# Kernel optimization log

Measured on AMD Instinct MI355X. Metric: run time of the kernel, lower is better.

Reference implementation:

```python
import jax, jax.numpy as jnp
import numpy as np

D_MODEL = 1024
D_STATE = 16
D_CONV = 4
EXPAND = 2
D_INNER = EXPAND * D_MODEL  # 2048
DT_RANK = (D_MODEL + 15) // 16  # 64
BATCH = 2
SEQ = 1024


def setup_inputs() -> dict:
    key = jax.random.key(0)
    ks = jax.random.split(key, 9)
    s = 0.02
    x = jax.random.normal(ks[0], (BATCH, SEQ, D_MODEL), jnp.float32)
    W_in = jax.random.normal(ks[1], (D_MODEL, 2 * D_INNER), jnp.float32) * s
    conv_w = jax.random.normal(ks[2], (D_INNER, D_CONV), jnp.float32) * s
    conv_b = jnp.zeros((D_INNER,), jnp.float32)
    W_x = jax.random.normal(ks[3], (D_INNER, DT_RANK + 2 * D_STATE), jnp.float32) * s
    W_dt = jax.random.normal(ks[4], (DT_RANK, D_INNER), jnp.float32) * (DT_RANK ** -0.5)
    # dt bias init: inverse softplus of dt ~ U(1e-3, 0.1)
    dt0 = jax.random.uniform(ks[5], (D_INNER,), jnp.float32, 1e-3, 0.1)
    b_dt = dt0 + jnp.log(-jnp.expm1(-dt0))
    # S4D-real A init: A[d, n] = -(n+1)
    A_log = jnp.log(jnp.tile(jnp.arange(1, D_STATE + 1, dtype=jnp.float32), (D_INNER, 1)))
    D_skip = jnp.ones((D_INNER,), jnp.float32)
    W_out = jax.random.normal(ks[6], (D_INNER, D_MODEL), jnp.float32) * s
    return {"x": x, "W_in": W_in, "conv_w": conv_w, "conv_b": conv_b,
            "W_x": W_x, "W_dt": W_dt, "b_dt": b_dt, "A_log": A_log,
            "D_skip": D_skip, "W_out": W_out}


def _mamba_forward(x, W_in, conv_w, conv_b, W_x, W_dt, b_dt, A_log, D_skip, W_out):
    Bsz, L, _ = x.shape
    # input projection -> [B, L, 2*d_inner], split into stream and gate
    xz = x @ W_in
    xr, z = jnp.split(xz, 2, axis=-1)
    # depthwise causal conv1d over time
    xt = xr.transpose(0, 2, 1)                       # [B, d_inner, L]
    kern = conv_w[:, None, :]                        # [d_inner, 1, d_conv]
    xc = jax.lax.conv_general_dilated(
        xt, kern, window_strides=(1,), padding=[(D_CONV - 1, 0)],
        feature_group_count=D_INNER, dimension_numbers=("NCH", "OIH", "NCH"))
    xc = jax.nn.silu(xc + conv_b[None, :, None]).transpose(0, 2, 1)  # [B, L, d_inner]
    # data-dependent dt, B, C
    dbl = xc @ W_x                                   # [B, L, dt_rank + 2*d_state]
    dt, Bm, Cm = jnp.split(dbl, [DT_RANK, DT_RANK + D_STATE], axis=-1)
    dt = jax.nn.softplus(dt @ W_dt + b_dt)           # [B, L, d_inner]
    A = -jnp.exp(A_log)                              # [d_inner, d_state]

    def step(h, inp):
        dt_t, B_t, C_t, x_t = inp                    # [B,d_inner],[B,d_state],[B,d_state],[B,d_inner]
        dA = jnp.exp(dt_t[..., None] * A)            # [B, d_inner, d_state]
        h = dA * h + (dt_t * x_t)[..., None] * B_t[:, None, :]
        y = jnp.einsum("bds,bs->bd", h, C_t)
        return h, y

    h0 = jnp.zeros((Bsz, D_INNER, D_STATE), x.dtype)
    xs = (dt.transpose(1, 0, 2), Bm.transpose(1, 0, 2),
          Cm.transpose(1, 0, 2), xc.transpose(1, 0, 2))
    _, ys = jax.lax.scan(step, h0, xs)               # ys: [L, B, d_inner]
    y = ys.transpose(1, 0, 2) + xc * D_skip
    y = y * jax.nn.silu(z)
    return y @ W_out                                 # [B, L, d_model]


def reference(x, W_in, conv_w, conv_b, W_x, W_dt, b_dt, A_log, D_skip, W_out):
    return _mamba_forward(x, W_in, conv_w, conv_b, W_x, W_dt, b_dt, A_log, D_skip, W_out)
```

## Files before the change

kernel.cpp:

```cpp
#include <hip/hip_runtime.h>

#define BATCH 2
#define SEQL 1024
#define DMODEL 1024
#define DINNER 2048
#define DSTATE 16
#define DTRANK 64
#define NCH 64
#define LC 16

typedef short bf16x8 __attribute__((ext_vector_type(8)));
typedef float f32x4 __attribute__((ext_vector_type(4)));
typedef int i32x4 __attribute__((ext_vector_type(4)));

__device__ __forceinline__ unsigned short f2bf(float f) {
  unsigned u = __float_as_uint(f);
  return (unsigned short)((u + 0x7fffu + ((u >> 16) & 1u)) >> 16);
}
__device__ __forceinline__ float bf2f(unsigned short u) {
  return __uint_as_float((unsigned)u << 16);
}
__device__ __forceinline__ float sigmoidf_(float x) { return 1.f / (1.f + __expf(-x)); }

__device__ __forceinline__ void gl_lds16(const unsigned short* g, unsigned short* l) {
  __builtin_amdgcn_global_load_lds(
      (const __attribute__((address_space(1))) unsigned int*)g,
      (__attribute__((address_space(3))) unsigned int*)l, 16, 0, 0);
}

#define BM 128
#define BN 128

__global__ __launch_bounds__(256) void k_gemm_mfma(
    const unsigned short* __restrict__ A,
    const unsigned short* __restrict__ Bt,
    float* __restrict__ C, unsigned short* __restrict__ C2,
    int M, int N, int K, const float* __restrict__ bias, int mode)
{
  __shared__ __attribute__((aligned(16))) unsigned short As[128 * 64];
  __shared__ __attribute__((aligned(16))) unsigned short Bs[128 * 64];
  const int tid = threadIdx.x;
  const int wave = tid >> 6, lane = tid & 63;
  const int m0 = blockIdx.x * BM, n0 = blockIdx.y * BN;
  const int Kc = K / gridDim.z;
  const int k0beg = blockIdx.z * Kc;
  float* Cz = C + (size_t)blockIdx.z * M * N;
  const int wr = (wave >> 1) * 64, wc = (wave & 1) * 64;
  const int fr = lane & 15;
  const int qw = lane >> 4;

  int srow[4], scol[4];
  #pragma unroll
  for (int i = 0; i < 4; ++i) {
    int off = wave * 4096 + i * 1024 + lane * 16;
    int row = off >> 7;
    int c16 = ((off >> 4) & 7) ^ (row & 7);
    srow[i] = row;
    scol[i] = c16 * 8;
  }

  f32x4 acc[4][4] = {};
  for (int k0 = k0beg; k0 < k0beg + Kc; k0 += 64) {
    #pragma unroll
    for (int i = 0; i < 4; ++i)
      gl_lds16(A + (size_t)(m0 + srow[i]) * K + k0 + scol[i],
               &As[(wave * 4096 + i * 1024) >> 1]);
    #pragma unroll
    for (int i = 0; i < 4; ++i)
      gl_lds16(Bt + (size_t)(n0 + srow[i]) * K + k0 + scol[i],
               &Bs[(wave * 4096 + i * 1024) >> 1]);
    __syncthreads();
    #pragma unroll
    for (int t = 0; t < 2; ++t) {
      bf16x8 af[4], bfv[4];
      #pragma unroll
      for (int i = 0; i < 4; ++i) {
        int row = wr + i * 16 + fr;
        int c16 = (t * 4 + qw) ^ (row & 7);
        af[i] = *(const bf16x8*)&As[row * 64 + c16 * 8];
      }
      #pragma unroll
      for (int j = 0; j < 4; ++j) {
        int row = wc + j * 16 + fr;
        int c16 = (t * 4 + qw) ^ (row & 7);
        bfv[j] = *(const bf16x8*)&Bs[row * 64 + c16 * 8];
      }
      #pragma unroll
      for (int i = 0; i < 4; ++i)
        #pragma unroll
        for (int j = 0; j < 4; ++j)
          acc[i][j] = __builtin_amdgcn_mfma_f32_16x16x32_bf16(af[i], bfv[j], acc[i][j], 0, 0, 0);
    }
    __syncthreads();
  }
  const int rr = qw * 4;
  if (mode == 1) {
    #pragma unroll
    for (int j = 0; j < 4; ++j) {
      float bj = bias[n0 + wc + j * 16 + fr];
      #pragma unroll
      for (int i = 0; i < 4; ++i)
        #pragma unroll
        for (int r = 0; r < 4; ++r) {
          float v = acc[i][j][r] + bj;
          C2[(size_t)(m0 + wr + i * 16 + rr + r) * N + (n0 + wc + j * 16 + fr)] =
              f2bf(__logf(1.f + __expf(v)));
        }
    }
  } else if (mode == 2) {
    if (n0 < 2048) {
      #pragma unroll
      for (int i = 0; i < 4; ++i)
        #pragma unroll
        for (int j = 0; j < 4; ++j)
          #pragma unroll
          for (int r = 0; r < 4; ++r)
            C[(size_t)(m0 + wr + i * 16 + rr + r) * 2048 + (n0 + wc + j * 16 + fr)] =
                acc[i][j][r];
    } else {
      #pragma unroll
      for (int i = 0; i < 4; ++i)
        #pragma unroll
        for (int j = 0; j < 4; ++j)
          #pragma unroll
          for (int r = 0; r < 4; ++r)
            C2[(size_t)(m0 + wr + i * 16 + rr + r) * 2048 + (n0 - 2048 + wc + j * 16 + fr)] =
                f2bf(acc[i][j][r]);
    }
  } else {
    #pragma unroll
    for (int i = 0; i < 4; ++i)
      #pragma unroll
      for (int j = 0; j < 4; ++j)
        #pragma unroll
        for (int r = 0; r < 4; ++r)
          Cz[(size_t)(m0 + wr + i * 16 + rr + r) * N + (n0 + wc + j * 16 + fr)] = acc[i][j][r];
  }
}

__device__ __forceinline__ void transpose_tile(
    const float* __restrict__ src, unsigned short* __restrict__ dst,
    int R, int C, int bx, int by, float* t )
{
  int bc = bx * 64, br = by * 64;
  int tr = threadIdx.x >> 2;
  int tc = (threadIdx.x & 3) * 16;
  #pragma unroll
  for (int i = 0; i < 4; ++i) {
    float4 v = *(const float4*)(src + (size_t)(br + tr) * C + bc + tc + i * 4);
    t[tr * 65 + tc + i * 4 + 0] = v.x; t[tr * 65 + tc + i * 4 + 1] = v.y;
    t[tr * 65 + tc + i * 4 + 2] = v.z; t[tr * 65 + tc + i * 4 + 3] = v.w;
  }
  __syncthreads();
  unsigned short tmp[16];
  #pragma unroll
  for (int i = 0; i < 16; ++i) tmp[i] = f2bf(t[(tc + i) * 65 + tr]);
  unsigned short* dp = dst + (size_t)(bc + tr) * R + br + tc;
  *(i32x4*)dp = *(i32x4*)&tmp[0];
  *(i32x4*)(dp + 8) = *(i32x4*)&tmp[8];
}

__global__ __launch_bounds__(256) void k_prep(
    const float* __restrict__ x,   unsigned short* __restrict__ xbf,
    const float* __restrict__ Win, unsigned short* __restrict__ wint,
    const float* __restrict__ Wout,unsigned short* __restrict__ woutt,
    const float* __restrict__ Wdt, unsigned short* __restrict__ wdtt,
    const float* __restrict__ Wx,  unsigned short* __restrict__ wxt)
{
  __shared__ float t[64 * 65];
  int bid = blockIdx.x;
  if (bid < 1024) {
    int i = (bid * 256 + threadIdx.x) * 8;
    float4 a = *(const float4*)(x + i);
    float4 b = *(const float4*)(x + i + 4);
    unsigned short tmp[8] = {f2bf(a.x), f2bf(a.y), f2bf(a.z), f2bf(a.w),
                             f2bf(b.x), f2bf(b.y), f2bf(b.z), f2bf(b.w)};
    *(i32x4*)(xbf + i) = *(i32x4*)tmp;
  } else if (bid < 2048) {
    int tt = bid - 1024;
    transpose_tile(Win, wint, 1024, 4096, tt & 63, tt >> 6, t);
  } else if (bid < 2560) {
    int tt = bid - 2048;
    transpose_tile(Wout, woutt, 2048, 1024, tt & 15, tt >> 4, t);
  } else if (bid < 2592) {
    int tt = bid - 2560;
    transpose_tile(Wdt, wdtt, 64, 2048, tt, 0, t);
  } else {
    int idx = (bid - 2592) * 256 + threadIdx.x;
    int k = idx & (DINNER - 1);
    int n = idx >> 11;
    float v = (n < 96) ? Wx[(size_t)k * 96 + n] : 0.f;
    wxt[idx] = f2bf(v);
  }
}

__global__ __launch_bounds__(256) void k_conv_silu(
    const float* __restrict__ xr, const float* __restrict__ cw,
    const float* __restrict__ cb, unsigned short* __restrict__ xcb)
{
  int idx = blockIdx.x * 256 + threadIdx.x;
  int d = idx & (DINNER - 1);
  int bl = idx >> 11;
  int l = bl & (SEQL - 1);
  float s = cb[d];
  #pragma unroll
  for (int k = 0; k < 4; ++k) {
    int ll = l - 3 + k;
    if (ll >= 0) s += xr[(size_t)(bl - 3 + k) * DINNER + d] * cw[d * 4 + k];
  }
  float r = s * sigmoidf_(s);
  xcb[idx] = f2bf(r);
}

__global__ void k_reduce2(const float* __restrict__ part, float* __restrict__ dbl,
                          unsigned short* __restrict__ dtraw)
{
  int idx = blockIdx.x * 256 + threadIdx.x;
  float s = 0.f;
  #pragma unroll
  for (int z = 0; z < 16; ++z) s += part[(size_t)z * 2048 * 128 + idx];
  dbl[idx] = s;
  int col = idx & 127, rw = idx >> 7;
  if (col < 64) dtraw[rw * 64 + col] = f2bf(s);
}

__global__ void k_reduce5(const float* __restrict__ part, float* __restrict__ out)
{
  int idx = (blockIdx.x * 256 + threadIdx.x) * 4;
  f32x4 s = *(const f32x4*)(part + idx);
  #pragma unroll
  for (int z = 1; z < 4; ++z)
    s += *(const f32x4*)(part + (size_t)z * 2048 * 1024 + idx);
  *(f32x4*)(out + idx) = s;
}

__global__ __launch_bounds__(256) void k_scan_A(
    const unsigned short* __restrict__ dtb, const unsigned short* __restrict__ xcb,
    const float* __restrict__ dbl, const float* __restrict__ Alog,
    float2* __restrict__ hpair)
{
  __shared__ __attribute__((aligned(16))) float bcB[LC][DSTATE];
  int gid = blockIdx.x * 256 + threadIdx.x;
  int d = gid & (DINNER - 1);
  int t = gid >> 11;
  int c = t & (NCH - 1);
  int b = t >> 6;
  const int r0 = b * SEQL + c * LC;
  bcB[threadIdx.x >> 4][threadIdx.x & 15] =
      dbl[(size_t)(r0 + (threadIdx.x >> 4)) * 128 + 64 + (threadIdx.x & 15)];
  float As[DSTATE];
  #pragma unroll
  for (int i = 0; i < 4; ++i) {
    f32x4 a = *(const f32x4*)&Alog[d * DSTATE + i * 4];
    #pragma unroll
    for (int j = 0; j < 4; ++j) As[i * 4 + j] = -__expf(a[j]);
  }
  __syncthreads();
  float h[DSTATE];
  #pragma unroll
  for (int s = 0; s < DSTATE; ++s) h[s] = 0.f;
  float sumdt = 0.f;
  #pragma unroll
  for (int li = 0; li < LC; li += 2) {
    float dt0 = bf2f(dtb[(size_t)(r0 + li) * DINNER + d]);
    float xv0 = bf2f(xcb[(size_t)(r0 + li) * DINNER + d]);
    float dt1 = bf2f(dtb[(size_t)(r0 + li + 1) * DINNER + d]);
    float xv1 = bf2f(xcb[(size_t)(r0 + li + 1) * DINNER + d]);
    f32x4 B0[4], B1[4];
    #pragma unroll
    for (int i = 0; i < 4; ++i) B0[i] = *(const f32x4*)&bcB[li][i * 4];
    #pragma unroll
    for (int i = 0; i < 4; ++i) B1[i] = *(const f32x4*)&bcB[li + 1][i * 4];
    float dtx0 = dt0 * xv0, dtx1 = dt1 * xv1;
    sumdt += dt0 + dt1;
    const float* Bv0 = (const float*)B0;
    const float* Bv1 = (const float*)B1;
    #pragma unroll
    for (int s = 0; s < DSTATE; ++s) {
      float dA0 = __expf(dt0 * As[s]);
      h[s] = dA0 * h[s] + dtx0 * Bv0[s];
      float dA1 = __expf(dt1 * As[s]);
      h[s] = dA1 * h[s] + dtx1 * Bv1[s];
    }
  }
  size_t base = ((size_t)(b * NCH + c) * DSTATE) * DINNER + d;
  #pragma unroll
  for (int s = 0; s < DSTATE; ++s) {
    float2 v; v.x = h[s]; v.y = __expf(sumdt * As[s]);
    hpair[base + (size_t)s * DINNER] = v;
  }
}

__global__ void k_scan_B(const float2* __restrict__ hpair, float* __restrict__ hin)
{
  int gid = blockIdx.x * 256 + threadIdx.x;
  int d = gid & (DINNER - 1);
  int s = (gid >> 11) & (DSTATE - 1);
  int b = gid >> 15;
  float h = 0.f;
  for (int c0 = 0; c0 < NCH; c0 += 8) {
    float2 v[8];
    #pragma unroll
    for (int i = 0; i < 8; ++i)
      v[i] = hpair[((size_t)(b * NCH + c0 + i) * DSTATE + s) * DINNER + d];
    #pragma unroll
    for (int i = 0; i < 8; ++i) {
      hin[((size_t)(b * NCH + c0 + i) * DSTATE + s) * DINNER + d] = h;
      h = v[i].y * h + v[i].x;
    }
  }
}

__global__ __launch_bounds__(256) void k_scan_C(
    const unsigned short* __restrict__ dtb, const unsigned short* __restrict__ xcb,
    const float* __restrict__ dbl, const float* __restrict__ Alog,
    const float* __restrict__ hin, const float* __restrict__ Dskip,
    const unsigned short* __restrict__ zb, unsigned short* __restrict__ yact)
{
  __shared__ __attribute__((aligned(16))) float bc[LC][32];
  int gid = blockIdx.x * 256 + threadIdx.x;
  int d = gid & (DINNER - 1);
  int t = gid >> 11;
  int c = t & (NCH - 1);
  int b = t >> 6;
  const int r0 = b * SEQL + c * LC;
  {
    int step = threadIdx.x >> 4, j = (threadIdx.x & 15) * 2;
    float2 v = *(const float2*)&dbl[(size_t)(r0 + step) * 128 + 64 + j];
    bc[step][j] = v.x; bc[step][j + 1] = v.y;
  }
  float As[DSTATE];
  #pragma unroll
  for (int i = 0; i < 4; ++i) {
    f32x4 a = *(const f32x4*)&Alog[d * DSTATE + i * 4];
    #pragma unroll
    for (int j = 0; j < 4; ++j) As[i * 4 + j] = -__expf(a[j]);
  }
  float h[DSTATE];
  size_t base = ((size_t)(b * NCH + c) * DSTATE) * DINNER + d;
  #pragma unroll
  for (int s = 0; s < DSTATE; ++s) h[s] = hin[base + (size_t)s * DINNER];
  const float dsk = Dskip[d];
  __syncthreads();
  #pragma unroll
  for (int li = 0; li < LC; li += 2) {
    const int r = r0 + li;
    float dt0 = bf2f(dtb[(size_t)r * DINNER + d]);
    float xv0 = bf2f(xcb[(size_t)r * DINNER + d]);
    float zv0 = bf2f(zb [(size_t)r * DINNER + d]);
    float dt1 = bf2f(dtb[(size_t)(r + 1) * DINNER + d]);
    float xv1 = bf2f(xcb[(size_t)(r + 1) * DINNER + d]);
    float zv1 = bf2f(zb [(size_t)(r + 1) * DINNER + d]);
    f32x4 B0[4], C0[4], B1[4], C1[4];
    #pragma unroll
    for (int i = 0; i < 4; ++i) B0[i] = *(const f32x4*)&bc[li][i * 4];
    #pragma unroll
    for (int i = 0; i < 4; ++i) C0[i] = *(const f32x4*)&bc[li][16 + i * 4];
    #pragma unroll
    for (int i = 0; i < 4; ++i) B1[i] = *(const f32x4*)&bc[li + 1][i * 4];
    #pragma unroll
    for (int i = 0; i < 4; ++i) C1[i] = *(const f32x4*)&bc[li + 1][16 + i * 4];
    const float* Bv0 = (const float*)B0; const float* Cv0 = (const float*)C0;
    const float* Bv1 = (const float*)B1; const float* Cv1 = (const float*)C1;
    float dtx0 = dt0 * xv0, dtx1 = dt1 * xv1;
    float y0 = 0.f, y1 = 0.f;
    #pragma unroll
    for (int s = 0; s < DSTATE; ++s) {
      float dA0 = __expf(dt0 * As[s]);
      h[s] = dA0 * h[s] + dtx0 * Bv0[s];
      y0 += h[s] * Cv0[s];
      float dA1 = __expf(dt1 * As[s]);
      h[s] = dA1 * h[s] + dtx1 * Bv1[s];
      y1 += h[s] * Cv1[s];
    }
    y0 += xv0 * dsk;
    y1 += xv1 * dsk;
    float ya0 = y0 * (zv0 * sigmoidf_(zv0));
    float ya1 = y1 * (zv1 * sigmoidf_(zv1));
    yact[(size_t)r * DINNER + d] = f2bf(ya0);
    yact[(size_t)(r + 1) * DINNER + d] = f2bf(ya1);
  }
}

extern "C" void kernel_launch(void* const* d_in, const int* in_sizes, int n_in,
                              void* d_out, int out_size, void* d_ws, size_t ws_size,
                              hipStream_t stream) {
  const float* x     = (const float*)d_in[0];
  const float* Win   = (const float*)d_in[1];
  const float* cw    = (const float*)d_in[2];
  const float* cbias = (const float*)d_in[3];
  const float* Wx    = (const float*)d_in[4];
  const float* Wdt   = (const float*)d_in[5];
  const float* bdt   = (const float*)d_in[6];
  const float* Alog  = (const float*)d_in[7];
  const float* Dsk   = (const float*)d_in[8];
  const float* Wout  = (const float*)d_in[9];
  float* out = (float*)d_out;

  char* ws = (char*)d_ws;
  const size_t MB = 1 << 20;
  float*          xr    = (float*)         (ws);
  unsigned short* xbf   = (unsigned short*)(ws + 16 * MB);
  unsigned short* wint  = (unsigned short*)(ws + 20 * MB);
  unsigned short* xcb   = (unsigned short*)(ws + 28 * MB);
  unsigned short* wxt   = (unsigned short*)(ws + 36 * MB);
  float*          dbl   = (float*)         (ws + 37 * MB);
  unsigned short* dtraw = (unsigned short*)(ws + 38 * MB);
  unsigned short* wdtt  = (unsigned short*)(ws + 39 * MB);
  unsigned short* dtb16 = (unsigned short*)(ws + 40 * MB);
  unsigned short* zb    = (unsigned short*)(ws + 48 * MB);
  float2*         hpair = (float2*)        (ws + 56 * MB);
  float*          hin   = (float*)         (ws + 88 * MB);
  unsigned short* yact  = (unsigned short*)(ws + 104 * MB);
  unsigned short* woutt = (unsigned short*)(ws + 112 * MB);
  float* part2 = (float*)(ws);
  float* part5 = (float*)(ws);
  (void)ws_size; (void)in_sizes; (void)n_in; (void)out_size;

  k_prep<<<3616, 256, 0, stream>>>(x, xbf, Win, wint, Wout, woutt, Wdt, wdtt, Wx, wxt);
  k_gemm_mfma<<<dim3(16, 32, 1), 256, 0, stream>>>(xbf, wint, xr, zb, 2048, 4096, 1024, nullptr, 2);
  k_conv_silu<<<16384, 256, 0, stream>>>(xr, cw, cbias, xcb);
  k_gemm_mfma<<<dim3(16, 1, 16), 256, 0, stream>>>(xcb, wxt, part2, nullptr, 2048, 128, 2048, nullptr, 0);
  k_reduce2<<<1024, 256, 0, stream>>>(part2, dbl, dtraw);
  k_gemm_mfma<<<dim3(16, 16, 1), 256, 0, stream>>>(dtraw, wdtt, nullptr, dtb16, 2048, 2048, 64, bdt, 1);
  k_scan_A<<<1024, 256, 0, stream>>>(dtb16, xcb, dbl, Alog, hpair);
  k_scan_B<<<256, 256, 0, stream>>>(hpair, hin);
  k_scan_C<<<1024, 256, 0, stream>>>(dtb16, xcb, dbl, Alog, hin, Dsk, zb, yact);
  k_gemm_mfma<<<dim3(16, 8, 4), 256, 0, stream>>>(yact, woutt, part5, nullptr, 2048, 1024, 2048, nullptr, 0);
  k_reduce5<<<2048, 256, 0, stream>>>(part5, out);
}
```

Baseline: 151.5 us.

## Store whole in-projection output as bf16 and use longer scan chunks

The in-projection GEMM now writes both the x and z halves as one bf16 [rows, 4096] buffer instead of fp32 x plus bf16 z. The conv and scan_C kernels read from that interleaved buffer. The chunked scan moves from 64 chunks of 16 steps to 32 chunks of 32 steps, which halves the chunk-state traffic and the work in the sequential pass, at the cost of fewer blocks and a partly unrolled inner loop. The workspace layout is reorganized to match. Rounding the conv input to bf16 adds some precision loss.

```diff
diff --git a/kernel.cpp b/kernel.cpp
--- a/kernel.cpp
+++ b/kernel.cpp
@@ -6,8 +6,8 @@
 #define DINNER 2048
 #define DSTATE 16
 #define DTRANK 64
-#define NCH 64
-#define LC 16
+#define NCH 32
+#define LC 32
 
 typedef short bf16x8 __attribute__((ext_vector_type(8)));
 typedef float f32x4 __attribute__((ext_vector_type(4)));
@@ -108,25 +108,14 @@
         }
     }
   } else if (mode == 2) {
-    if (n0 < 2048) {
-      #pragma unroll
-      for (int i = 0; i < 4; ++i)
+    #pragma unroll
+    for (int i = 0; i < 4; ++i)
+      #pragma unroll
+      for (int j = 0; j < 4; ++j)
         #pragma unroll
-        for (int j = 0; j < 4; ++j)
-          #pragma unroll
-          for (int r = 0; r < 4; ++r)
-            C[(size_t)(m0 + wr + i * 16 + rr + r) * 2048 + (n0 + wc + j * 16 + fr)] =
-                acc[i][j][r];
-    } else {
-      #pragma unroll
-      for (int i = 0; i < 4; ++i)
-        #pragma unroll
-        for (int j = 0; j < 4; ++j)
-          #pragma unroll
-          for (int r = 0; r < 4; ++r)
-            C2[(size_t)(m0 + wr + i * 16 + rr + r) * 2048 + (n0 - 2048 + wc + j * 16 + fr)] =
-                f2bf(acc[i][j][r]);
-    }
+        for (int r = 0; r < 4; ++r)
+          C2[(size_t)(m0 + wr + i * 16 + rr + r) * N + (n0 + wc + j * 16 + fr)] =
+              f2bf(acc[i][j][r]);
   } else {
     #pragma unroll
     for (int i = 0; i < 4; ++i)
@@ -195,7 +184,7 @@
 }
 
 __global__ __launch_bounds__(256) void k_conv_silu(
-    const float* __restrict__ xr, const float* __restrict__ cw,
+    const unsigned short* __restrict__ xzb, const float* __restrict__ cw,
     const float* __restrict__ cb, unsigned short* __restrict__ xcb)
 {
   int idx = blockIdx.x * 256 + threadIdx.x;
@@ -206,7 +195,7 @@
   #pragma unroll
   for (int k = 0; k < 4; ++k) {
     int ll = l - 3 + k;
-    if (ll >= 0) s += xr[(size_t)(bl - 3 + k) * DINNER + d] * cw[d * 4 + k];
+    if (ll >= 0) s += bf2f(xzb[(size_t)(bl - 3 + k) * 4096 + d]) * cw[d * 4 + k];
   }
   float r = s * sigmoidf_(s);
   xcb[idx] = f2bf(r);
@@ -244,10 +233,12 @@
   int d = gid & (DINNER - 1);
   int t = gid >> 11;
   int c = t & (NCH - 1);
-  int b = t >> 6;
+  int b = t >> 5;
   const int r0 = b * SEQL + c * LC;
-  bcB[threadIdx.x >> 4][threadIdx.x & 15] =
-      dbl[(size_t)(r0 + (threadIdx.x >> 4)) * 128 + 64 + (threadIdx.x & 15)];
+  for (int i = threadIdx.x; i < LC * DSTATE; i += 256) {
+    int step = i >> 4, col = i & 15;
+    bcB[step][col] = dbl[(size_t)(r0 + step) * 128 + 64 + col];
+  }
   float As[DSTATE];
   #pragma unroll
   for (int i = 0; i < 4; ++i) {
@@ -260,7 +251,7 @@
   #pragma unroll
   for (int s = 0; s < DSTATE; ++s) h[s] = 0.f;
   float sumdt = 0.f;
-  #pragma unroll
+  #pragma unroll 4
   for (int li = 0; li < LC; li += 2) {
     float dt0 = bf2f(dtb[(size_t)(r0 + li) * DINNER + d]);
     float xv0 = bf2f(xcb[(size_t)(r0 + li) * DINNER + d]);
@@ -315,19 +306,18 @@
     const unsigned short* __restrict__ dtb, const unsigned short* __restrict__ xcb,
     const float* __restrict__ dbl, const float* __restrict__ Alog,
     const float* __restrict__ hin, const float* __restrict__ Dskip,
-    const unsigned short* __restrict__ zb, unsigned short* __restrict__ yact)
+    const unsigned short* __restrict__ xzb, unsigned short* __restrict__ yact)
 {
   __shared__ __attribute__((aligned(16))) float bc[LC][32];
   int gid = blockIdx.x * 256 + threadIdx.x;
   int d = gid & (DINNER - 1);
   int t = gid >> 11;
   int c = t & (NCH - 1);
-  int b = t >> 6;
+  int b = t >> 5;
   const int r0 = b * SEQL + c * LC;
-  {
-    int step = threadIdx.x >> 4, j = (threadIdx.x & 15) * 2;
-    float2 v = *(const float2*)&dbl[(size_t)(r0 + step) * 128 + 64 + j];
-    bc[step][j] = v.x; bc[step][j + 1] = v.y;
+  for (int i = threadIdx.x; i < LC * 32; i += 256) {
+    int step = i >> 5, j = i & 31;
+    bc[step][j] = dbl[(size_t)(r0 + step) * 128 + 64 + j];
   }
   float As[DSTATE];
   #pragma unroll
@@ -342,15 +332,15 @@
   for (int s = 0; s < DSTATE; ++s) h[s] = hin[base + (size_t)s * DINNER];
   const float dsk = Dskip[d];
   __syncthreads();
-  #pragma unroll
+  #pragma unroll 4
   for (int li = 0; li < LC; li += 2) {
     const int r = r0 + li;
     float dt0 = bf2f(dtb[(size_t)r * DINNER + d]);
     float xv0 = bf2f(xcb[(size_t)r * DINNER + d]);
-    float zv0 = bf2f(zb [(size_t)r * DINNER + d]);
+    float zv0 = bf2f(xzb[(size_t)r * 4096 + 2048 + d]);
     float dt1 = bf2f(dtb[(size_t)(r + 1) * DINNER + d]);
     float xv1 = bf2f(xcb[(size_t)(r + 1) * DINNER + d]);
-    float zv1 = bf2f(zb [(size_t)(r + 1) * DINNER + d]);
+    float zv1 = bf2f(xzb[(size_t)(r + 1) * 4096 + 2048 + d]);
     f32x4 B0[4], C0[4], B1[4], C1[4];
     #pragma unroll
     for (int i = 0; i < 4; ++i) B0[i] = *(const f32x4*)&bc[li][i * 4];
@@ -399,7 +389,7 @@
 
   char* ws = (char*)d_ws;
   const size_t MB = 1 << 20;
-  float*          xr    = (float*)         (ws);
+  unsigned short* xzb   = (unsigned short*)(ws);
   unsigned short* xbf   = (unsigned short*)(ws + 16 * MB);
   unsigned short* wint  = (unsigned short*)(ws + 20 * MB);
   unsigned short* xcb   = (unsigned short*)(ws + 28 * MB);
@@ -408,24 +398,23 @@
   unsigned short* dtraw = (unsigned short*)(ws + 38 * MB);
   unsigned short* wdtt  = (unsigned short*)(ws + 39 * MB);
   unsigned short* dtb16 = (unsigned short*)(ws + 40 * MB);
-  unsigned short* zb    = (unsigned short*)(ws + 48 * MB);
-  float2*         hpair = (float2*)        (ws + 56 * MB);
-  float*          hin   = (float*)         (ws + 88 * MB);
-  unsigned short* yact  = (unsigned short*)(ws + 104 * MB);
-  unsigned short* woutt = (unsigned short*)(ws + 112 * MB);
-  float* part2 = (float*)(ws);
-  float* part5 = (float*)(ws);
+  float2*         hpair = (float2*)        (ws + 48 * MB);
+  float*          hin   = (float*)         (ws + 64 * MB);
+  unsigned short* yact  = (unsigned short*)(ws + 72 * MB);
+  unsigned short* woutt = (unsigned short*)(ws + 80 * MB);
+  float*          part2 = (float*)         (ws + 84 * MB);
+  float*          part5 = (float*)         (ws + 100 * MB);
   (void)ws_size; (void)in_sizes; (void)n_in; (void)out_size;
 
   k_prep<<<3616, 256, 0, stream>>>(x, xbf, Win, wint, Wout, woutt, Wdt, wdtt, Wx, wxt);
-  k_gemm_mfma<<<dim3(16, 32, 1), 256, 0, stream>>>(xbf, wint, xr, zb, 2048, 4096, 1024, nullptr, 2);
-  k_conv_silu<<<16384, 256, 0, stream>>>(xr, cw, cbias, xcb);
+  k_gemm_mfma<<<dim3(16, 32, 1), 256, 0, stream>>>(xbf, wint, nullptr, xzb, 2048, 4096, 1024, nullptr, 2);
+  k_conv_silu<<<16384, 256, 0, stream>>>(xzb, cw, cbias, xcb);
   k_gemm_mfma<<<dim3(16, 1, 16), 256, 0, stream>>>(xcb, wxt, part2, nullptr, 2048, 128, 2048, nullptr, 0);
   k_reduce2<<<1024, 256, 0, stream>>>(part2, dbl, dtraw);
   k_gemm_mfma<<<dim3(16, 16, 1), 256, 0, stream>>>(dtraw, wdtt, nullptr, dtb16, 2048, 2048, 64, bdt, 1);
-  k_scan_A<<<1024, 256, 0, stream>>>(dtb16, xcb, dbl, Alog, hpair);
+  k_scan_A<<<512, 256, 0, stream>>>(dtb16, xcb, dbl, Alog, hpair);
   k_scan_B<<<256, 256, 0, stream>>>(hpair, hin);
-  k_scan_C<<<1024, 256, 0, stream>>>(dtb16, xcb, dbl, Alog, hin, Dsk, zb, yact);
+  k_scan_C<<<512, 256, 0, stream>>>(dtb16, xcb, dbl, Alog, hin, Dsk, xzb, yact);
   k_gemm_mfma<<<dim3(16, 8, 4), 256, 0, stream>>>(yact, woutt, part5, nullptr, 2048, 1024, 2048, nullptr, 0);
   k_reduce5<<<2048, 256, 0, stream>>>(part5, out);
 }
```

New measurement: 154.3 us. About the same (+1.9%).
